# Performance work log

Measured on AMD Instinct MI355X. Metric: run time of the kernel, lower is better.

## Reference

```python
import jax, jax.numpy as jnp
import numpy as np

EPS = 1e-12

def _l2n(v):
    return v / (jnp.linalg.norm(v) + EPS)

def _sn(w, u, v):
    """One power iteration of spectral norm. w: [out, in] (1x1 conv flattened).
    u, v updates carry no gradient (requires_grad=False in torch); sigma grads flow through w."""
    v1 = jax.lax.stop_gradient(_l2n(w.T @ u))
    u1 = jax.lax.stop_gradient(_l2n(w @ v1))
    sigma = u1 @ (w @ v1)
    return w / sigma

def setup_inputs() -> dict:
    key = jax.random.key(0)
    ks = jax.random.split(key, 16)
    B, C, H, W = 4, 64, 64, 64
    d_qk, d_v = C // 8, C // 2
    inp = {
        "x": jax.random.normal(ks[0], (B, C, H, W), dtype=jnp.float32),
        "w_theta": jax.random.normal(ks[1], (d_qk, C), dtype=jnp.float32) * 0.05,
        "w_phi": jax.random.normal(ks[2], (d_qk, C), dtype=jnp.float32) * 0.05,
        "w_g": jax.random.normal(ks[3], (d_v, C), dtype=jnp.float32) * 0.05,
        "w_o": jax.random.normal(ks[4], (C, d_v), dtype=jnp.float32) * 0.05,
        "gamma": jax.random.normal(ks[5], (1,), dtype=jnp.float32),
        "u_theta": _l2n(jax.random.normal(ks[6], (d_qk,), dtype=jnp.float32)),
        "v_theta": _l2n(jax.random.normal(ks[7], (C,), dtype=jnp.float32)),
        "u_phi": _l2n(jax.random.normal(ks[8], (d_qk,), dtype=jnp.float32)),
        "v_phi": _l2n(jax.random.normal(ks[9], (C,), dtype=jnp.float32)),
        "u_g": _l2n(jax.random.normal(ks[10], (d_v,), dtype=jnp.float32)),
        "v_g": _l2n(jax.random.normal(ks[11], (C,), dtype=jnp.float32)),
        "u_o": _l2n(jax.random.normal(ks[12], (C,), dtype=jnp.float32)),
        "v_o": _l2n(jax.random.normal(ks[13], (d_v,), dtype=jnp.float32)),
    }
    return inp

def reference(x, w_theta, w_phi, w_g, w_o, gamma,
              u_theta, v_theta, u_phi, v_phi, u_g, v_g, u_o, v_o):
    B, C, H, W = x.shape
    HW = H * W
    wt = _sn(w_theta, u_theta, v_theta)
    wp = _sn(w_phi, u_phi, v_phi)
    wg = _sn(w_g, u_g, v_g)
    wo = _sn(w_o, u_o, v_o)
    xf = x.reshape(B, C, HW)                      # [B, C, N]
    theta = jnp.einsum('oc,bcn->bon', wt, xf)     # [B, C/8, N]
    phi = jnp.einsum('oc,bcn->bon', wp, xf)       # [B, C/8, N]
    g = jnp.einsum('oc,bcn->bon', wg, xf)         # [B, C/2, N]
    scores = jnp.einsum('bci,bcj->bij', theta, phi)  # [B, N, N]
    beta = jax.nn.softmax(scores, axis=1)            # softmax over dim=1 (rows), as in torch code
    o = jnp.einsum('bci,bij->bcj', g, beta)          # [B, C/2, N]
    out = jnp.einsum('oc,bcn->bon', wo, o).reshape(B, C, H, W)
    return gamma.reshape(()) * out + x
```

## Files before the change

### kernel.cpp

```cpp
#include <hip/hip_runtime.h>
#include <math.h>

#define N     4096
#define B     4
#define C     64
#define DQK   8
#define DV    32
#define LOG2E 1.4426950408889634f
#define PROJ_BLOCKS ((B * 3 * N) / 256)

typedef __attribute__((ext_vector_type(8)))  short  short8;
typedef __attribute__((ext_vector_type(16))) float  float16;

union U4S8 { int4 v; unsigned int u[4]; short8 s; };

__device__ __forceinline__ unsigned short f2bf(float f) {
  union { float f; unsigned int u; } c; c.f = f;
  unsigned int r = c.u + 0x7FFF + ((c.u >> 16) & 1);
  return (unsigned short)(r >> 16);
}
__device__ __forceinline__ float bf2f(unsigned short h) {
  union { unsigned int u; float f; } c; c.u = ((unsigned int)h) << 16;
  return c.f;
}
__device__ __forceinline__ unsigned int fbits(float f) {
  union { float f; unsigned int u; } c; c.f = f; return c.u;
}
__device__ __forceinline__ int bitswap23(int n) {
  return (n & ~0xC) | ((n & 4) << 1) | ((n & 8) >> 1);
}

__global__ __launch_bounds__(256) void projsig_kernel(
    const float* __restrict__ x,
    const float* __restrict__ w_theta, const float* __restrict__ w_phi,
    const float* __restrict__ w_g,     const float* __restrict__ w_o,
    const float* __restrict__ u_theta, const float* __restrict__ u_phi,
    const float* __restrict__ u_g,     const float* __restrict__ u_o,
    float* __restrict__ scales,
    unsigned short* __restrict__ theta_bf,
    unsigned short* __restrict__ phi_bf,
    unsigned short* __restrict__ v_pack) {
  __shared__ float v1[64];
  int bid = blockIdx.x;
  int tid = threadIdx.x;

  if (bid >= PROJ_BLOCKS) {
    int which = bid - PROJ_BLOCKS;
    const float* w; const float* u; int M, K;
    if      (which == 0) { w = w_theta; u = u_theta; M = DQK; K = C;  }
    else if (which == 1) { w = w_phi;   u = u_phi;   M = DQK; K = C;  }
    else if (which == 2) { w = w_g;     u = u_g;     M = DV;  K = C;  }
    else                 { w = w_o;     u = u_o;     M = C;   K = DV; }

    float acc = 0.f;
    if (tid < K) {
      for (int m = 0; m < M; ++m) acc += w[m * K + tid] * u[m];
    }
    float ss = acc * acc;
    #pragma unroll
    for (int off = 32; off; off >>= 1) ss += __shfl_xor(ss, off);
    float nrm = sqrtf(ss);
    if (tid < 64) v1[tid] = (tid < K) ? acc / (nrm + 1e-12f) : 0.f;
    __syncthreads();

    float t = 0.f;
    if (tid < M) {
      for (int k = 0; k < K; ++k) t += w[tid * K + k] * v1[k];
    }
    float ts = t * t;
    #pragma unroll
    for (int off = 32; off; off >>= 1) ts += __shfl_xor(ts, off);
    float tn = sqrtf(ts);
    if (tid == 0) scales[which] = (tn + 1e-12f) / ts;
    return;
  }

  int t  = bid * 256 + tid;
  int n  = t & (N - 1);
  int bk = t >> 12;
  int kind = bk % 3;
  int b    = bk / 3;

  const float* xp = x + (size_t)b * C * N + n;
  float xv[C];
  #pragma unroll
  for (int c = 0; c < C; ++c) xv[c] = xp[(size_t)c * N];

  float o[16];
  if (kind == 0) {
    #pragma unroll
    for (int r = 0; r < 8; ++r) {
      const float* wr = w_theta + r * C;
      float a = 0.f;
      #pragma unroll
      for (int c = 0; c < C; ++c) a += wr[c] * xv[c];
      o[r] = a;
    }
    #pragma unroll
    for (int r = 0; r < 8; ++r) {
      const float* wr = w_phi + r * C;
      float a = 0.f;
      #pragma unroll
      for (int c = 0; c < C; ++c) a += wr[c] * xv[c];
      o[8 + r] = a;
    }
    U4S8 pt, pp;
    #pragma unroll
    for (int i = 0; i < 4; ++i) {
      pt.u[i] = ((unsigned int)f2bf(o[2 * i])) |
                ((unsigned int)f2bf(o[2 * i + 1]) << 16);
      pp.u[i] = ((unsigned int)f2bf(o[8 + 2 * i])) |
                ((unsigned int)f2bf(o[8 + 2 * i + 1]) << 16);
    }
    *(int4*)(theta_bf + ((size_t)b * N + n) * 8) = pt.v;
    *(int4*)(phi_bf   + ((size_t)b * N + n) * 8) = pp.v;
  } else {
    int c0base = (kind - 1) * 16;
    const float* wb = w_g + c0base * C;
    #pragma unroll
    for (int r = 0; r < 16; ++r) {
      const float* wr = wb + r * C;
      float a = 0.f;
      #pragma unroll
      for (int c = 0; c < C; ++c) a += wr[c] * xv[c];
      o[r] = a;
    }
    int m  = bitswap23(n);
    int q  = m >> 4;
    int hf = (m >> 3) & 1;
    int ii = m & 7;
    unsigned short* dst = v_pack + ((size_t)(b * 256 + q)) * 64 * 8;
    #pragma unroll
    for (int r = 0; r < 16; ++r) {
      int lane = (c0base + r) | (hf << 5);
      dst[lane * 8 + ii] = f2bf(o[r]);
    }
  }
}

__global__ __launch_bounds__(512) void attn_kernel(
    const unsigned short* __restrict__ theta_bf,
    const unsigned short* __restrict__ phi_bf,
    const unsigned short* __restrict__ v_pack,
    const float* __restrict__ w_o, const float* __restrict__ scales,
    const float* __restrict__ gamma,
    const float* __restrict__ x, float* __restrict__ out) {
  __shared__ float po_lds[8][16][64];
  __shared__ float l_lds[8][32];
  __shared__ float Lrcp[32];
  __shared__ float ot[DV][33];
  __shared__ float wsh[C * DV];

  int bi = blockIdx.x;
  int qt = bi & 127;
  int b  = bi >> 7;
  int tid  = threadIdx.x;
  int lane = tid & 63;
  int wav  = tid >> 6;
  int half = lane >> 5;
  int l31  = lane & 31;
  int j    = qt * 32 + l31;

  float kappa = scales[0] * scales[1] * LOG2E;
  float swo   = scales[2] * scales[3] * gamma[0];
  for (int i = tid; i < C * DV; i += 512) wsh[i] = w_o[i] * swo;

  U4S8 phu; phu.u[0] = phu.u[1] = phu.u[2] = phu.u[3] = 0;
  if (half == 0) {
    U4S8 raw; raw.v = *(const int4*)(phi_bf + ((size_t)b * N + j) * 8);
    #pragma unroll
    for (int i = 0; i < 8; ++i)
      phu.s[i] = (short)f2bf(bf2f((unsigned short)raw.s[i]) * kappa);
  }
  short8 phB = phu.s;

  float16 z16;
  #pragma unroll
  for (int r = 0; r < 16; ++r) z16[r] = 0.f;

  float ls0 = 0.f, ls1 = 0.f, ls2 = 0.f, ls3 = 0.f;
  float16 o;
  #pragma unroll
  for (int r = 0; r < 16; ++r) o[r] = 0.f;

  int kstart = wav * 512;

  #pragma unroll 2
  for (int tt = 0; tt < 16; ++tt) {
    int kb = kstart + tt * 32;
    int q1 = kb >> 4;

    U4S8 ta;  ta.v  = *(const int4*)(theta_bf + ((size_t)b * N + kb + l31) * 8);
    const int4* vp = (const int4*)(v_pack + ((size_t)(b * 256 + q1)) * 64 * 8);
    U4S8 va1; va1.v = vp[lane];
    U4S8 va2; va2.v = vp[64 + lane];

    float16 sf = __builtin_amdgcn_mfma_f32_32x32x16_bf16(ta.s, phB, z16, 0, 0, 0);

    float p[16];
    #pragma unroll
    for (int r = 0; r < 16; ++r)
      p[r] = __builtin_amdgcn_exp2f(sf[r]);
    #pragma unroll
    for (int r = 0; r < 16; r += 4) {
      ls0 += p[r];
      ls1 += p[r + 1];
      ls2 += p[r + 2];
      ls3 += p[r + 3];
    }

    unsigned int pk[8];
    #pragma unroll
    for (int i = 0; i < 8; ++i)
      pk[i] = __builtin_amdgcn_perm(fbits(p[2 * i + 1]), fbits(p[2 * i]),
                                    0x07060302u);
    U4S8 b1, b2;
    b1.u[0] = pk[0]; b1.u[1] = pk[1]; b1.u[2] = pk[2]; b1.u[3] = pk[3];
    b2.u[0] = pk[4]; b2.u[1] = pk[5]; b2.u[2] = pk[6]; b2.u[3] = pk[7];

    o = __builtin_amdgcn_mfma_f32_32x32x16_bf16(va1.s, b1.s, o, 0, 0, 0);
    o = __builtin_amdgcn_mfma_f32_32x32x16_bf16(va2.s, b2.s, o, 0, 0, 0);
  }

  float lsum = (ls0 + ls1) + (ls2 + ls3);

  lsum += __shfl_xor(lsum, 32);
  if (half == 0) l_lds[wav][l31] = lsum;
  #pragma unroll
  for (int r = 0; r < 16; ++r)
    po_lds[wav][r][lane] = o[r];
  __syncthreads();

  int cell0 = tid;
  int cell1 = tid + 512;
  int rr0 = cell0 >> 6, ii0 = cell0 & 63;
  int rr1 = cell1 >> 6, ii1 = cell1 & 63;
  float ov0 = 0.f, ov1 = 0.f;
  #pragma unroll
  for (int w = 0; w < 8; ++w) {
    ov0 += po_lds[w][rr0][ii0];
    ov1 += po_lds[w][rr1][ii1];
  }
  if (tid < 32) {
    float L = 0.f;
    #pragma unroll
    for (int w = 0; w < 8; ++w) L += l_lds[w][tid];
    Lrcp[tid] = 1.f / L;
  }
  __syncthreads();

  {
    int cc0 = (rr0 & 3) + 8 * (rr0 >> 2) + 4 * (ii0 >> 5);
    int jq0 = ii0 & 31;
    ot[cc0][jq0] = ov0 * Lrcp[jq0];
    int cc1 = (rr1 & 3) + 8 * (rr1 >> 2) + 4 * (ii1 >> 5);
    int jq1 = ii1 & 31;
    ot[cc1][jq1] = ov1 * Lrcp[jq1];
  }
  __syncthreads();

  int j2  = tid & 31;
  int ocp = tid >> 5;
  float a0 = 0.f, a1 = 0.f, a2 = 0.f, a3 = 0.f;
  #pragma unroll
  for (int c = 0; c < DV; ++c) {
    float ov = ot[c][j2];
    a0 = fmaf(wsh[(ocp     ) * DV + c], ov, a0);
    a1 = fmaf(wsh[(ocp + 16) * DV + c], ov, a1);
    a2 = fmaf(wsh[(ocp + 32) * DV + c], ov, a2);
    a3 = fmaf(wsh[(ocp + 48) * DV + c], ov, a3);
  }
  size_t base = (size_t)b * C * N + (size_t)qt * 32 + j2;
  out[base + (size_t)(ocp     ) * N] = a0 + x[base + (size_t)(ocp     ) * N];
  out[base + (size_t)(ocp + 16) * N] = a1 + x[base + (size_t)(ocp + 16) * N];
  out[base + (size_t)(ocp + 32) * N] = a2 + x[base + (size_t)(ocp + 32) * N];
  out[base + (size_t)(ocp + 48) * N] = a3 + x[base + (size_t)(ocp + 48) * N];
}

extern "C" void kernel_launch(void* const* d_in, const int* in_sizes, int n_in,
                              void* d_out, int out_size, void* d_ws, size_t ws_size,
                              hipStream_t stream) {
  const float* x       = (const float*)d_in[0];
  const float* w_theta = (const float*)d_in[1];
  const float* w_phi   = (const float*)d_in[2];
  const float* w_g     = (const float*)d_in[3];
  const float* w_o     = (const float*)d_in[4];
  const float* gamma   = (const float*)d_in[5];
  const float* u_theta = (const float*)d_in[6];
  const float* u_phi   = (const float*)d_in[8];
  const float* u_g     = (const float*)d_in[10];
  const float* u_o     = (const float*)d_in[12];
  float* out = (float*)d_out;

  float* ws = (float*)d_ws;
  float*          scales   = ws;
  unsigned short* theta_bf = (unsigned short*)(ws + 16);
  unsigned short* phi_bf   = theta_bf + (size_t)B * N * 8;
  unsigned short* v_pack   = phi_bf   + (size_t)B * N * 8;

  projsig_kernel<<<PROJ_BLOCKS + 4, 256, 0, stream>>>(
      x, w_theta, w_phi, w_g, w_o, u_theta, u_phi, u_g, u_o,
      scales, theta_bf, phi_bf, v_pack);
  attn_kernel<<<B * 128, 512, 0, stream>>>(
      theta_bf, phi_bf, v_pack, w_o, scales, gamma, x, out);
}
```

Measured before the change: 117.4 us.

## Process two 32-column query tiles per attention block to reuse K/V loads

Each attention block now handles 64 output columns instead of 32, so every theta and v_pack tile loaded from global memory feeds two score and PV MFMA chains. This halves the grid to 256 blocks and halves the redundant K/V traffic per output column. The cost is twice the accumulator registers and LDS (po_lds grows to 64KB), which can lower occupancy. With 256 blocks there may be under one block per CU on a 256-CU device.

```diff
diff --git a/kernel.cpp b/kernel.cpp
--- a/kernel.cpp
+++ b/kernel.cpp
@@ -145,43 +145,50 @@
     const float* __restrict__ w_o, const float* __restrict__ scales,
     const float* __restrict__ gamma,
     const float* __restrict__ x, float* __restrict__ out) {
-  __shared__ float po_lds[8][16][64];
-  __shared__ float l_lds[8][32];
-  __shared__ float Lrcp[32];
-  __shared__ float ot[DV][33];
+  __shared__ float po_lds[8][32][64];
+  __shared__ float l_lds[8][64];
+  __shared__ float Lrcp[64];
+  __shared__ float ot[DV][65];
   __shared__ float wsh[C * DV];
 
   int bi = blockIdx.x;
-  int qt = bi & 127;
-  int b  = bi >> 7;
+  int qt = bi & 63;
+  int b  = bi >> 6;
   int tid  = threadIdx.x;
   int lane = tid & 63;
   int wav  = tid >> 6;
   int half = lane >> 5;
   int l31  = lane & 31;
-  int j    = qt * 32 + l31;
+  int j0   = qt * 64 + l31;
+  int j1   = j0 + 32;
 
   float kappa = scales[0] * scales[1] * LOG2E;
   float swo   = scales[2] * scales[3] * gamma[0];
   for (int i = tid; i < C * DV; i += 512) wsh[i] = w_o[i] * swo;
 
-  U4S8 phu; phu.u[0] = phu.u[1] = phu.u[2] = phu.u[3] = 0;
+  U4S8 ph0; ph0.u[0] = ph0.u[1] = ph0.u[2] = ph0.u[3] = 0;
+  U4S8 ph1; ph1.u[0] = ph1.u[1] = ph1.u[2] = ph1.u[3] = 0;
   if (half == 0) {
-    U4S8 raw; raw.v = *(const int4*)(phi_bf + ((size_t)b * N + j) * 8);
-    #pragma unroll
-    for (int i = 0; i < 8; ++i)
-      phu.s[i] = (short)f2bf(bf2f((unsigned short)raw.s[i]) * kappa);
-  }
-  short8 phB = phu.s;
+    U4S8 r0; r0.v = *(const int4*)(phi_bf + ((size_t)b * N + j0) * 8);
+    U4S8 r1; r1.v = *(const int4*)(phi_bf + ((size_t)b * N + j1) * 8);
+    #pragma unroll
+    for (int i = 0; i < 8; ++i) {
+      ph0.s[i] = (short)f2bf(bf2f((unsigned short)r0.s[i]) * kappa);
+      ph1.s[i] = (short)f2bf(bf2f((unsigned short)r1.s[i]) * kappa);
+    }
+  }
+  short8 phB0 = ph0.s;
+  short8 phB1 = ph1.s;
 
   float16 z16;
   #pragma unroll
   for (int r = 0; r < 16; ++r) z16[r] = 0.f;
 
-  float ls0 = 0.f, ls1 = 0.f, ls2 = 0.f, ls3 = 0.f;
-  float16 o;
-  #pragma unroll
-  for (int r = 0; r < 16; ++r) o[r] = 0.f;
+  float lsA0 = 0.f, lsA1 = 0.f;
+  float lsB0 = 0.f, lsB1 = 0.f;
+  float16 o0, o1;
+  #pragma unroll
+  for (int r = 0; r < 16; ++r) { o0[r] = 0.f; o1[r] = 0.f; }
 
   int kstart = wav * 512;
 
@@ -195,53 +202,80 @@
     U4S8 va1; va1.v = vp[lane];
     U4S8 va2; va2.v = vp[64 + lane];
 
-    float16 sf = __builtin_amdgcn_mfma_f32_32x32x16_bf16(ta.s, phB, z16, 0, 0, 0);
-
-    float p[16];
+    float16 sf0 = __builtin_amdgcn_mfma_f32_32x32x16_bf16(ta.s, phB0, z16, 0, 0, 0);
+    float p0[16];
     #pragma unroll
     for (int r = 0; r < 16; ++r)
-      p[r] = __builtin_amdgcn_exp2f(sf[r]);
-    #pragma unroll
-    for (int r = 0; r < 16; r += 4) {
-      ls0 += p[r];
-      ls1 += p[r + 1];
-      ls2 += p[r + 2];
-      ls3 += p[r + 3];
-    }
-
-    unsigned int pk[8];
+      p0[r] = __builtin_amdgcn_exp2f(sf0[r]);
+    #pragma unroll
+    for (int r = 0; r < 16; r += 2) {
+      lsA0 += p0[r];
+      lsA1 += p0[r + 1];
+    }
+    unsigned int pk0[8];
     #pragma unroll
     for (int i = 0; i < 8; ++i)
-      pk[i] = __builtin_amdgcn_perm(fbits(p[2 * i + 1]), fbits(p[2 * i]),
-                                    0x07060302u);
+      pk0[i] = __builtin_amdgcn_perm(fbits(p0[2 * i + 1]), fbits(p0[2 * i]),
+                                     0x07060302u);
     U4S8 b1, b2;
-    b1.u[0] = pk[0]; b1.u[1] = pk[1]; b1.u[2] = pk[2]; b1.u[3] = pk[3];
-    b2.u[0] = pk[4]; b2.u[1] = pk[5]; b2.u[2] = pk[6]; b2.u[3] = pk[7];
-
-    o = __builtin_amdgcn_mfma_f32_32x32x16_bf16(va1.s, b1.s, o, 0, 0, 0);
-    o = __builtin_amdgcn_mfma_f32_32x32x16_bf16(va2.s, b2.s, o, 0, 0, 0);
-  }
-
-  float lsum = (ls0 + ls1) + (ls2 + ls3);
-
-  lsum += __shfl_xor(lsum, 32);
-  if (half == 0) l_lds[wav][l31] = lsum;
-  #pragma unroll
-  for (int r = 0; r < 16; ++r)
-    po_lds[wav][r][lane] = o[r];
+    b1.u[0] = pk0[0]; b1.u[1] = pk0[1]; b1.u[2] = pk0[2]; b1.u[3] = pk0[3];
+    b2.u[0] = pk0[4]; b2.u[1] = pk0[5]; b2.u[2] = pk0[6]; b2.u[3] = pk0[7];
+    o0 = __builtin_amdgcn_mfma_f32_32x32x16_bf16(va1.s, b1.s, o0, 0, 0, 0);
+    o0 = __builtin_amdgcn_mfma_f32_32x32x16_bf16(va2.s, b2.s, o0, 0, 0, 0);
+
+    float16 sf1 = __builtin_amdgcn_mfma_f32_32x32x16_bf16(ta.s, phB1, z16, 0, 0, 0);
+    float p1[16];
+    #pragma unroll
+    for (int r = 0; r < 16; ++r)
+      p1[r] = __builtin_amdgcn_exp2f(sf1[r]);
+    #pragma unroll
+    for (int r = 0; r < 16; r += 2) {
+      lsB0 += p1[r];
+      lsB1 += p1[r + 1];
+    }
+    unsigned int pk1[8];
+    #pragma unroll
+    for (int i = 0; i < 8; ++i)
+      pk1[i] = __builtin_amdgcn_perm(fbits(p1[2 * i + 1]), fbits(p1[2 * i]),
+                                     0x07060302u);
+    U4S8 c1, c2;
+    c1.u[0] = pk1[0]; c1.u[1] = pk1[1]; c1.u[2] = pk1[2]; c1.u[3] = pk1[3];
+    c2.u[0] = pk1[4]; c2.u[1] = pk1[5]; c2.u[2] = pk1[6]; c2.u[3] = pk1[7];
+    o1 = __builtin_amdgcn_mfma_f32_32x32x16_bf16(va1.s, c1.s, o1, 0, 0, 0);
+    o1 = __builtin_amdgcn_mfma_f32_32x32x16_bf16(va2.s, c2.s, o1, 0, 0, 0);
+  }
+
+  float lsum0 = lsA0 + lsA1;
+  float lsum1 = lsB0 + lsB1;
+
+  lsum0 += __shfl_xor(lsum0, 32);
+  lsum1 += __shfl_xor(lsum1, 32);
+  if (half == 0) {
+    l_lds[wav][l31]      = lsum0;
+    l_lds[wav][32 + l31] = lsum1;
+  }
+  #pragma unroll
+  for (int r = 0; r < 16; ++r) {
+    po_lds[wav][r][lane]      = o0[r];
+    po_lds[wav][16 + r][lane] = o1[r];
+  }
   __syncthreads();
 
-  int cell0 = tid;
-  int cell1 = tid + 512;
-  int rr0 = cell0 >> 6, ii0 = cell0 & 63;
-  int rr1 = cell1 >> 6, ii1 = cell1 & 63;
-  float ov0 = 0.f, ov1 = 0.f;
-  #pragma unroll
-  for (int w = 0; w < 8; ++w) {
-    ov0 += po_lds[w][rr0][ii0];
-    ov1 += po_lds[w][rr1][ii1];
-  }
-  if (tid < 32) {
+  float ov0 = 0.f, ov1 = 0.f, ov2 = 0.f, ov3 = 0.f;
+  {
+    int R0 = tid >> 6,          ii0 = tid & 63;
+    int R1 = (tid + 512) >> 6,  ii1 = tid & 63;
+    int R2 = (tid + 1024) >> 6, ii2 = tid & 63;
+    int R3 = (tid + 1536) >> 6, ii3 = tid & 63;
+    #pragma unroll
+    for (int w = 0; w < 8; ++w) {
+      ov0 += po_lds[w][R0][ii0];
+      ov1 += po_lds[w][R1][ii1];
+      ov2 += po_lds[w][R2][ii2];
+      ov3 += po_lds[w][R3][ii3];
+    }
+  }
+  if (tid < 64) {
     float L = 0.f;
     #pragma unroll
     for (int w = 0; w < 8; ++w) L += l_lds[w][tid];
@@ -250,31 +284,45 @@
   __syncthreads();
 
   {
-    int cc0 = (rr0 & 3) + 8 * (rr0 >> 2) + 4 * (ii0 >> 5);
-    int jq0 = ii0 & 31;
-    ot[cc0][jq0] = ov0 * Lrcp[jq0];
-    int cc1 = (rr1 & 3) + 8 * (rr1 >> 2) + 4 * (ii1 >> 5);
-    int jq1 = ii1 & 31;
-    ot[cc1][jq1] = ov1 * Lrcp[jq1];
+    int ii = tid & 63;
+    #pragma unroll
+    for (int k = 0; k < 4; ++k) {
+      int R  = (tid + 512 * k) >> 6;
+      float ov = (k == 0) ? ov0 : (k == 1) ? ov1 : (k == 2) ? ov2 : ov3;
+      int qs = R >> 4;
+      int r  = R & 15;
+      int cc = (r & 3) + 8 * (r >> 2) + 4 * (ii >> 5);
+      int jq = (ii & 31) + 32 * qs;
+      ot[cc][jq] = ov * Lrcp[jq];
+    }
   }
   __syncthreads();
 
-  int j2  = tid & 31;
-  int ocp = tid >> 5;
+  int j2  = tid & 63;
+  int ocp = tid >> 6;
   float a0 = 0.f, a1 = 0.f, a2 = 0.f, a3 = 0.f;
+  float a4 = 0.f, a5 = 0.f, a6 = 0.f, a7 = 0.f;
   #pragma unroll
   for (int c = 0; c < DV; ++c) {
     float ov = ot[c][j2];
     a0 = fmaf(wsh[(ocp     ) * DV + c], ov, a0);
-    a1 = fmaf(wsh[(ocp + 16) * DV + c], ov, a1);
-    a2 = fmaf(wsh[(ocp + 32) * DV + c], ov, a2);
-    a3 = fmaf(wsh[(ocp + 48) * DV + c], ov, a3);
-  }
-  size_t base = (size_t)b * C * N + (size_t)qt * 32 + j2;
+    a1 = fmaf(wsh[(ocp +  8) * DV + c], ov, a1);
+    a2 = fmaf(wsh[(ocp + 16) * DV + c], ov, a2);
+    a3 = fmaf(wsh[(ocp + 24) * DV + c], ov, a3);
+    a4 = fmaf(wsh[(ocp + 32) * DV + c], ov, a4);
+    a5 = fmaf(wsh[(ocp + 40) * DV + c], ov, a5);
+    a6 = fmaf(wsh[(ocp + 48) * DV + c], ov, a6);
+    a7 = fmaf(wsh[(ocp + 56) * DV + c], ov, a7);
+  }
+  size_t base = (size_t)b * C * N + (size_t)qt * 64 + j2;
   out[base + (size_t)(ocp     ) * N] = a0 + x[base + (size_t)(ocp     ) * N];
-  out[base + (size_t)(ocp + 16) * N] = a1 + x[base + (size_t)(ocp + 16) * N];
-  out[base + (size_t)(ocp + 32) * N] = a2 + x[base + (size_t)(ocp + 32) * N];
-  out[base + (size_t)(ocp + 48) * N] = a3 + x[base + (size_t)(ocp + 48) * N];
+  out[base + (size_t)(ocp +  8) * N] = a1 + x[base + (size_t)(ocp +  8) * N];
+  out[base + (size_t)(ocp + 16) * N] = a2 + x[base + (size_t)(ocp + 16) * N];
+  out[base + (size_t)(ocp + 24) * N] = a3 + x[base + (size_t)(ocp + 24) * N];
+  out[base + (size_t)(ocp + 32) * N] = a4 + x[base + (size_t)(ocp + 32) * N];
+  out[base + (size_t)(ocp + 40) * N] = a5 + x[base + (size_t)(ocp + 40) * N];
+  out[base + (size_t)(ocp + 48) * N] = a6 + x[base + (size_t)(ocp + 48) * N];
+  out[base + (size_t)(ocp + 56) * N] = a7 + x[base + (size_t)(ocp + 56) * N];
 }
 
 extern "C" void kernel_launch(void* const* d_in, const int* in_sizes, int n_in,
@@ -301,6 +349,6 @@
   projsig_kernel<<<PROJ_BLOCKS + 4, 256, 0, stream>>>(
       x, w_theta, w_phi, w_g, w_o, u_theta, u_phi, u_g, u_o,
       scales, theta_bf, phi_bf, v_pack);
-  attn_kernel<<<B * 128, 512, 0, stream>>>(
+  attn_kernel<<<B * 64, 512, 0, stream>>>(
       theta_bf, phi_bf, v_pack, w_o, scales, gamma, x, out);
 }
```

Measured after the change: 114.3 us. 2.7% less time.
